# Optimization experiments

Measured on AMD Instinct MI355X. Metric: run time of the kernel, lower is better.

Reference implementation:

```python
import jax, jax.numpy as jnp
import numpy as np

B, S, D, H = 2, 2048, 1024, 16
DK = D // H  # 64


def setup_inputs() -> dict:
    key = jax.random.key(0)
    ks = jax.random.split(key, 12)
    def lin(kw, kb, fan_in, shape_w):
        bound = 1.0 / np.sqrt(fan_in)
        W = jax.random.uniform(kw, shape_w, jnp.float32, -bound, bound)
        b = jax.random.uniform(kb, (shape_w[0],), jnp.float32, -bound, bound)
        return W, b
    Q = jax.random.normal(ks[0], (B, S, D), jnp.float32)
    K = jax.random.normal(ks[1], (B, S, D), jnp.float32)
    V = jax.random.normal(ks[2], (B, S, D), jnp.float32)
    attn_mask = jax.random.randint(ks[3], (B, S, S), 0, 2) == 1  # bool, True=masked
    Wq, bq = lin(ks[4], ks[5], D, (D, D))
    Wk, bk = lin(ks[6], ks[7], D, (D, D))
    Wv, bv = lin(ks[8], ks[9], D, (D, D))
    Wo, bo = lin(ks[10], ks[11], D, (D, D))
    return {"Q": Q, "K": K, "V": V, "attn_mask": attn_mask,
            "Wq": Wq, "bq": bq, "Wk": Wk, "bk": bk,
            "Wv": Wv, "bv": bv, "Wo": Wo, "bo": bo}


def reference(Q, K, V, attn_mask, Wq, bq, Wk, bk, Wv, bv, Wo, bo):
    b, s, d = Q.shape
    # project and split heads: [B,S,D] -> [B,H,S,DK]
    def heads(x, W, bias):
        y = x @ W.T + bias
        return y.reshape(b, -1, H, DK).transpose(0, 2, 1, 3)
    q = heads(Q, Wq, bq)
    k = heads(K, Wk, bk)
    v = heads(V, Wv, bv)
    # scaled dot-product attention with custom reweighting
    scores = jnp.einsum('bhqd,bhkd->bhqk', q, k) / np.sqrt(DK).astype(jnp.float32)
    scores = jnp.where(attn_mask[:, None, :, :], jnp.float32(-1e9), scores)
    attn_weights = jax.nn.softmax(scores, axis=-1) * scores.shape[-1]  # non-standard *S_k scale
    ctx = jnp.einsum('bhqk,bhkd->bhqd', attn_weights, v)
    ctx = ctx.transpose(0, 2, 1, 3).reshape(b, -1, H * DK)
    output = ctx @ Wo.T + bo
    return output, attn_weights
```

## Files before the change

kernel.cpp:

```cpp
#include <hip/hip_runtime.h>
#include <hip/hip_bf16.h>
#include <type_traits>

typedef __bf16 bf16_t;
typedef __attribute__((ext_vector_type(8))) __bf16 bf16x8;
typedef __attribute__((ext_vector_type(4))) float f32x4;

#define B_ 2
#define S_ 2048
#define D_ 1024
#define H_ 16
#define DK_ 64

enum { OM_F32 = 0, OM_BF16 = 1, OM_SPLIT = 2, OM_HEADT = 3 };

__device__ inline void split8(const float* __restrict__ p, bf16x8& h, bf16x8& l) {
    float4 x0 = *(const float4*)p;
    float4 x1 = *(const float4*)(p + 4);
    float xs[8] = {x0.x, x0.y, x0.z, x0.w, x1.x, x1.y, x1.z, x1.w};
#pragma unroll
    for (int i = 0; i < 8; ++i) {
        bf16_t hh = (bf16_t)xs[i];
        h[i] = hh;
        l[i] = (bf16_t)(xs[i] - (float)hh);
    }
}
__device__ inline void hi8(const float* __restrict__ p, bf16x8& h) {
    float4 x0 = *(const float4*)p;
    float4 x1 = *(const float4*)(p + 4);
    float xs[8] = {x0.x, x0.y, x0.z, x0.w, x1.x, x1.y, x1.z, x1.w};
#pragma unroll
    for (int i = 0; i < 8; ++i) h[i] = (bf16_t)xs[i];
}

template <typename AT, int OMODE, bool SPLIT>
__global__ __launch_bounds__(256) void gemm_bt(
    const AT* __restrict__ A,
    const float* __restrict__ W,
    const float* __restrict__ bias,
    void* __restrict__ Yp,
    void* __restrict__ Y2p,
    int M, int N, int K)
{
    const int NB = N >> 6;
    const int bm = blockIdx.x / NB;
    const int bn = blockIdx.x % NB;
    const int tid  = threadIdx.x;
    const int wave = tid >> 6;
    const int lane = tid & 63;
    const int l16  = lane & 15;
    const int quad = lane >> 4;
    const int wm = wave >> 1, wn = wave & 1;

    __shared__ bf16_t Ah[64][40];
    __shared__ bf16_t Wh[64][40];
    __shared__ bf16_t Al[SPLIT ? 64 : 1][40];
    __shared__ bf16_t Wl[SPLIT ? 64 : 1][40];
    __shared__ bf16_t T[OMODE == OM_HEADT ? 64 : 1][72];

    const int srow = tid >> 2;
    const int scol = (tid & 3) * 8;

    f32x4 acc[2][2];
#pragma unroll
    for (int i = 0; i < 2; ++i)
#pragma unroll
        for (int j = 0; j < 2; ++j) acc[i][j] = (f32x4){0.f, 0.f, 0.f, 0.f};

    const AT*    Arow = A + (size_t)(bm * 64 + srow) * K + scol;
    const float* Wrow = W + (size_t)(bn * 64 + srow) * K + scol;

    for (int k0 = 0; k0 < K; k0 += 32) {
        if constexpr (std::is_same_v<AT, float>) {
            bf16x8 ah, al;
            if constexpr (SPLIT) {
                split8(Arow + k0, ah, al);
                *(bf16x8*)(&Al[srow][scol]) = al;
            } else {
                hi8(Arow + k0, ah);
            }
            *(bf16x8*)(&Ah[srow][scol]) = ah;
        } else {
            *(bf16x8*)(&Ah[srow][scol]) = *(const bf16x8*)(Arow + k0);
        }
        {
            bf16x8 wh, wl;
            if constexpr (SPLIT) {
                split8(Wrow + k0, wh, wl);
                *(bf16x8*)(&Wl[srow][scol]) = wl;
            } else {
                hi8(Wrow + k0, wh);
            }
            *(bf16x8*)(&Wh[srow][scol]) = wh;
        }
        __syncthreads();

        bf16x8 afh[2], bfh[2], afl[2], bfl[2];
#pragma unroll
        for (int mi = 0; mi < 2; ++mi) {
            afh[mi] = *(const bf16x8*)(&Ah[wm * 32 + mi * 16 + l16][quad * 8]);
            if constexpr (SPLIT)
                afl[mi] = *(const bf16x8*)(&Al[wm * 32 + mi * 16 + l16][quad * 8]);
        }
#pragma unroll
        for (int ni = 0; ni < 2; ++ni) {
            bfh[ni] = *(const bf16x8*)(&Wh[wn * 32 + ni * 16 + l16][quad * 8]);
            if constexpr (SPLIT)
                bfl[ni] = *(const bf16x8*)(&Wl[wn * 32 + ni * 16 + l16][quad * 8]);
        }

#pragma unroll
        for (int mi = 0; mi < 2; ++mi)
#pragma unroll
            for (int ni = 0; ni < 2; ++ni) {
                acc[mi][ni] = __builtin_amdgcn_mfma_f32_16x16x32_bf16(
                    afh[mi], bfh[ni], acc[mi][ni], 0, 0, 0);
                if constexpr (SPLIT) {
                    acc[mi][ni] = __builtin_amdgcn_mfma_f32_16x16x32_bf16(
                        afl[mi], bfh[ni], acc[mi][ni], 0, 0, 0);
                    acc[mi][ni] = __builtin_amdgcn_mfma_f32_16x16x32_bf16(
                        afh[mi], bfl[ni], acc[mi][ni], 0, 0, 0);
                }
            }
        __syncthreads();
    }

    if constexpr (OMODE == OM_HEADT) {
#pragma unroll
        for (int ni = 0; ni < 2; ++ni) {
            const int cl = wn * 32 + ni * 16 + l16;
            const float bv = bias[bn * 64 + cl];
#pragma unroll
            for (int mi = 0; mi < 2; ++mi)
#pragma unroll
                for (int r = 0; r < 4; ++r) {
                    const int rl = wm * 32 + mi * 16 + quad * 4 + r;
                    T[cl][rl] = (bf16_t)(acc[mi][ni][r] + bv);
                }
        }
        __syncthreads();
        const int bb  = bm >> 5;
        const int ss0 = (bm * 64) & (S_ - 1);
#pragma unroll
        for (int it = 0; it < 2; ++it) {
            const int dk = it * 32 + (tid >> 3);
            const int so = (tid & 7) * 8;
            *(bf16x8*)((bf16_t*)Yp +
                ((size_t)((bb * H_ + bn) * DK_ + dk) << 11) + ss0 + so) =
                *(const bf16x8*)(&T[dk][so]);
        }
        return;
    }

#pragma unroll
    for (int ni = 0; ni < 2; ++ni) {
        const int col = bn * 64 + wn * 32 + ni * 16 + l16;
        const float bv = bias[col];
#pragma unroll
        for (int mi = 0; mi < 2; ++mi) {
#pragma unroll
            for (int r = 0; r < 4; ++r) {
                const int row = bm * 64 + wm * 32 + mi * 16 + quad * 4 + r;
                const float v = acc[mi][ni][r] + bv;
                if constexpr (OMODE == OM_F32) {
                    ((float*)Yp)[(size_t)row * N + col] = v;
                } else if constexpr (OMODE == OM_BF16) {
                    ((bf16_t*)Yp)[(size_t)row * N + col] = (bf16_t)v;
                } else if constexpr (OMODE == OM_SPLIT) {
                    const bf16_t hh = (bf16_t)v;
                    ((bf16_t*)Yp)[(size_t)row * N + col] = hh;
                    ((bf16_t*)Y2p)[(size_t)row * N + col] = (bf16_t)(v - (float)hh);
                }
            }
        }
    }
}

__global__ __launch_bounds__(256) void pack_mask(
    const int* __restrict__ mask,
    unsigned long long* __restrict__ pk)
{
    const size_t nwords = (size_t)B_ * S_ * S_ / 64;
    const int lane = threadIdx.x & 63;
    size_t w = (size_t)blockIdx.x * 4 + (threadIdx.x >> 6);
    const size_t stride = (size_t)gridDim.x * 4;
    for (; w < nwords; w += stride) {
        const int m = mask[w * 64 + lane];
        const unsigned long long bb = __ballot(m != 0);
        if (lane == 0) pk[w] = bb;
    }
}

__global__ __launch_bounds__(256) void attn_scores(
    const bf16_t* __restrict__ qh_g,
    const bf16_t* __restrict__ ql_g,
    const bf16_t* __restrict__ kh_g,
    const bf16_t* __restrict__ kl_g,
    const unsigned long long* __restrict__ pm,
    float* __restrict__ wout,
    float* __restrict__ normbuf)
{
    const int bid = blockIdx.x;
    const int qt = bid & 31;
    const int h  = (bid >> 5) & 15;
    const int b  = bid >> 9;
    const int tid  = threadIdx.x;
    const int wave = tid >> 6;
    const int lane = tid & 63;
    const int l16  = lane & 15;
    const int quad = lane >> 4;

    const int q0 = qt * 64 + wave * 16;

    __shared__ bf16_t Kh[64][72];
    __shared__ bf16_t Kl[64][72];

    const size_t qoff = ((size_t)(b * S_ + q0 + l16)) * D_ + h * DK_ + quad * 8;
    const bf16x8 qh0 = *(const bf16x8*)(qh_g + qoff);
    const bf16x8 qh1 = *(const bf16x8*)(qh_g + qoff + 32);
    const bf16x8 ql0 = *(const bf16x8*)(ql_g + qoff);
    const bf16x8 ql1 = *(const bf16x8*)(ql_g + qoff + 32);

    const float scale = 0.125f;

    const int srow = tid >> 2;
    const int scol = (tid & 3) * 16;
    const bf16_t* khst = kh_g + (size_t)b * S_ * D_ + h * DK_;
    const bf16_t* klst = kl_g + (size_t)b * S_ * D_ + h * DK_;

    const unsigned long long* pmrow = pm + (size_t)b * S_ * (S_ / 64);
    const size_t wbase = ((size_t)(b * H_ + h)) * S_ * S_;

    float lsum[4] = {0.f, 0.f, 0.f, 0.f};

    for (int j0 = 0; j0 < S_; j0 += 64) {
        {
            const size_t ko = (size_t)(j0 + srow) * D_ + scol;
            *(bf16x8*)(&Kh[srow][scol])     = *(const bf16x8*)(khst + ko);
            *(bf16x8*)(&Kh[srow][scol + 8]) = *(const bf16x8*)(khst + ko + 8);
            *(bf16x8*)(&Kl[srow][scol])     = *(const bf16x8*)(klst + ko);
            *(bf16x8*)(&Kl[srow][scol + 8]) = *(const bf16x8*)(klst + ko + 8);
        }
        unsigned long long mw[4];
#pragma unroll
        for (int r = 0; r < 4; ++r) {
            const int q = q0 + quad * 4 + r;
            mw[r] = pmrow[(size_t)q * (S_ / 64) + (j0 >> 6)];
        }
        __syncthreads();

#pragma unroll
        for (int sub = 0; sub < 4; ++sub) {
            const int rr = sub * 16 + l16;
            const bf16x8 kh0 = *(const bf16x8*)(&Kh[rr][quad * 8]);
            const bf16x8 kh1 = *(const bf16x8*)(&Kh[rr][32 + quad * 8]);
            const bf16x8 kl0 = *(const bf16x8*)(&Kl[rr][quad * 8]);
            const bf16x8 kl1 = *(const bf16x8*)(&Kl[rr][32 + quad * 8]);
            f32x4 c = (f32x4){0.f, 0.f, 0.f, 0.f};
            c = __builtin_amdgcn_mfma_f32_16x16x32_bf16(qh0, kh0, c, 0, 0, 0);
            c = __builtin_amdgcn_mfma_f32_16x16x32_bf16(qh1, kh1, c, 0, 0, 0);
            c = __builtin_amdgcn_mfma_f32_16x16x32_bf16(ql0, kh0, c, 0, 0, 0);
            c = __builtin_amdgcn_mfma_f32_16x16x32_bf16(ql1, kh1, c, 0, 0, 0);
            c = __builtin_amdgcn_mfma_f32_16x16x32_bf16(qh0, kl0, c, 0, 0, 0);
            c = __builtin_amdgcn_mfma_f32_16x16x32_bf16(qh1, kl1, c, 0, 0, 0);
            const int jt = j0 + sub * 16;
#pragma unroll
            for (int r = 0; r < 4; ++r) {
                const int q = q0 + quad * 4 + r;
                const int msk = (int)((mw[r] >> (sub * 16 + l16)) & 1ull);
                const float e = msk ? 0.f : __expf(c[r] * scale);
                lsum[r] += e;
                __builtin_nontemporal_store(e, &wout[wbase + (size_t)q * S_ + jt + l16]);
            }
        }
        __syncthreads();
    }

#pragma unroll
    for (int r = 0; r < 4; ++r) {
        float v = lsum[r];
        v += __shfl_xor(v, 1);
        v += __shfl_xor(v, 2);
        v += __shfl_xor(v, 4);
        v += __shfl_xor(v, 8);
        lsum[r] = v;
    }
    if (l16 == 0) {
#pragma unroll
        for (int r = 0; r < 4; ++r)
            normbuf[(size_t)(b * H_ + h) * S_ + q0 + quad * 4 + r] = 2048.f / lsum[r];
    }
}

__global__ __launch_bounds__(256) void attn_pv(
    const bf16_t* __restrict__ vt_g,
    const float*  __restrict__ normbuf,
    float* __restrict__ wout,
    bf16_t* __restrict__ ctx)
{
    const int bid = blockIdx.x;
    const int qt = bid & 31;
    const int h  = (bid >> 5) & 15;
    const int b  = bid >> 9;
    const int tid  = threadIdx.x;
    const int wave = tid >> 6;
    const int lane = tid & 63;
    const int l16  = lane & 15;
    const int quad = lane >> 4;

    const int q0 = qt * 64 + wave * 16;

    __shared__ bf16_t vT[64][72];

    const int sdk = tid >> 2;
    const int sjo = (tid & 3) * 16;
    const bf16_t* vtst = vt_g + ((size_t)(b * H_ + h) * DK_ + sdk) * S_ + sjo;

    const size_t wbase = ((size_t)(b * H_ + h)) * S_ * S_;
    const float nrmA = normbuf[(size_t)(b * H_ + h) * S_ + q0 + l16];
    float norm_c[4];
#pragma unroll
    for (int r = 0; r < 4; ++r)
        norm_c[r] = normbuf[(size_t)(b * H_ + h) * S_ + q0 + quad * 4 + r];

    f32x4 acc[4];
#pragma unroll
    for (int t = 0; t < 4; ++t) acc[t] = (f32x4){0.f, 0.f, 0.f, 0.f};

    float* wrow = wout + wbase + (size_t)(q0 + l16) * S_;

    for (int j0 = 0; j0 < S_; j0 += 64) {
        {
            *(bf16x8*)(&vT[sdk][sjo])     = *(const bf16x8*)(vtst + j0);
            *(bf16x8*)(&vT[sdk][sjo + 8]) = *(const bf16x8*)(vtst + j0 + 8);
        }
        __syncthreads();

#pragma unroll
        for (int half = 0; half < 2; ++half) {
            const int jj = j0 + half * 32 + quad * 8;
            float* ep = wrow + jj;
            float4 e0, e1;
            e0.x = __builtin_nontemporal_load(ep + 0);
            e0.y = __builtin_nontemporal_load(ep + 1);
            e0.z = __builtin_nontemporal_load(ep + 2);
            e0.w = __builtin_nontemporal_load(ep + 3);
            e1.x = __builtin_nontemporal_load(ep + 4);
            e1.y = __builtin_nontemporal_load(ep + 5);
            e1.z = __builtin_nontemporal_load(ep + 6);
            e1.w = __builtin_nontemporal_load(ep + 7);
            const float es[8] = {e0.x, e0.y, e0.z, e0.w, e1.x, e1.y, e1.z, e1.w};
            bf16x8 wa;
#pragma unroll
            for (int i = 0; i < 8; ++i) {
                __builtin_nontemporal_store(es[i] * nrmA, ep + i);
                wa[i] = (bf16_t)es[i];
            }
#pragma unroll
            for (int t = 0; t < 4; ++t) {
                const bf16x8 vf = *(const bf16x8*)(&vT[t * 16 + l16][half * 32 + quad * 8]);
                acc[t] = __builtin_amdgcn_mfma_f32_16x16x32_bf16(wa, vf, acc[t], 0, 0, 0);
            }
        }
        __syncthreads();
    }

#pragma unroll
    for (int t = 0; t < 4; ++t) {
#pragma unroll
        for (int r = 0; r < 4; ++r) {
            const int q = q0 + quad * 4 + r;
            ctx[((size_t)(b * S_ + q)) * D_ + h * DK_ + t * 16 + l16] =
                (bf16_t)(acc[t][r] * norm_c[r]);
        }
    }
}

extern "C" void kernel_launch(void* const* d_in, const int* in_sizes, int n_in,
                              void* d_out, int out_size, void* d_ws, size_t ws_size,
                              hipStream_t stream) {
    const float* Q    = (const float*)d_in[0];
    const float* K    = (const float*)d_in[1];
    const float* V    = (const float*)d_in[2];
    const int*   mask = (const int*)d_in[3];
    const float* Wq   = (const float*)d_in[4];
    const float* bq   = (const float*)d_in[5];
    const float* Wk   = (const float*)d_in[6];
    const float* bk   = (const float*)d_in[7];
    const float* Wv   = (const float*)d_in[8];
    const float* bv   = (const float*)d_in[9];
    const float* Wo   = (const float*)d_in[10];
    const float* bo   = (const float*)d_in[11];

    const size_t BSD = (size_t)B_ * S_ * D_;
    float* out  = (float*)d_out;
    float* wout = out + BSD;

    bf16_t* qh = (bf16_t*)d_ws;
    bf16_t* ql = qh + BSD;
    bf16_t* kh = ql + BSD;
    bf16_t* kl = kh + BSD;
    bf16_t* vt = kl + BSD;
    bf16_t* cx = vt + BSD;
    unsigned long long* pk = (unsigned long long*)(cx + BSD);
    float* normbuf = (float*)(pk + (size_t)B_ * S_ * (S_ / 64));

    const int M = B_ * S_;
    const int N = D_;
    const int Kd = D_;
    const dim3 ggrid((M / 64) * (N / 64));
    const dim3 gblk(256);

    pack_mask<<<dim3(512), gblk, 0, stream>>>(mask, pk);

    gemm_bt<float, OM_SPLIT, true><<<ggrid, gblk, 0, stream>>>(Q, Wq, bq, qh, ql, M, N, Kd);
    gemm_bt<float, OM_SPLIT, true><<<ggrid, gblk, 0, stream>>>(K, Wk, bk, kh, kl, M, N, Kd);
    gemm_bt<float, OM_HEADT, false><<<ggrid, gblk, 0, stream>>>(V, Wv, bv, vt, nullptr, M, N, Kd);

    attn_scores<<<dim3(B_ * H_ * (S_ / 64)), gblk, 0, stream>>>(
        qh, ql, kh, kl, pk, wout, normbuf);

    attn_pv<<<dim3(B_ * H_ * (S_ / 64)), gblk, 0, stream>>>(
        vt, normbuf, wout, cx);

    gemm_bt<bf16_t, OM_F32, false><<<ggrid, gblk, 0, stream>>>(cx, Wo, bo, out, nullptr, M, N, Kd);
}
```

Baseline: 1.130 ms.

## Fuse attention scores and PV into two-pass kernel recomputing QK

```diff
diff --git a/kernel.cpp b/kernel.cpp
--- a/kernel.cpp
+++ b/kernel.cpp
@@ -191,14 +191,15 @@
     }
 }
 
-__global__ __launch_bounds__(256) void attn_scores(
+__global__ __launch_bounds__(256) void attn_kernel(
     const bf16_t* __restrict__ qh_g,
     const bf16_t* __restrict__ ql_g,
     const bf16_t* __restrict__ kh_g,
     const bf16_t* __restrict__ kl_g,
+    const bf16_t* __restrict__ vt_g,
     const unsigned long long* __restrict__ pm,
     float* __restrict__ wout,
-    float* __restrict__ normbuf)
+    bf16_t* __restrict__ ctx)
 {
     const int bid = blockIdx.x;
     const int qt = bid & 31;
@@ -214,6 +215,8 @@
 
     __shared__ bf16_t Kh[64][72];
     __shared__ bf16_t Kl[64][72];
+    __shared__ bf16_t vT[64][72];
+    __shared__ bf16_t wl[4][16][72];
 
     const size_t qoff = ((size_t)(b * S_ + q0 + l16)) * D_ + h * DK_ + quad * 8;
     const bf16x8 qh0 = *(const bf16x8*)(qh_g + qoff);
@@ -227,6 +230,7 @@
     const int scol = (tid & 3) * 16;
     const bf16_t* khst = kh_g + (size_t)b * S_ * D_ + h * DK_;
     const bf16_t* klst = kl_g + (size_t)b * S_ * D_ + h * DK_;
+    const bf16_t* vtst = vt_g + ((size_t)(b * H_ + h) * DK_ + srow) * S_ + scol;
 
     const unsigned long long* pmrow = pm + (size_t)b * S_ * (S_ / 64);
     const size_t wbase = ((size_t)(b * H_ + h)) * S_ * S_;
@@ -240,6 +244,64 @@
             *(bf16x8*)(&Kh[srow][scol + 8]) = *(const bf16x8*)(khst + ko + 8);
             *(bf16x8*)(&Kl[srow][scol])     = *(const bf16x8*)(klst + ko);
             *(bf16x8*)(&Kl[srow][scol + 8]) = *(const bf16x8*)(klst + ko + 8);
+        }
+        unsigned long long mw[4];
+#pragma unroll
+        for (int r = 0; r < 4; ++r) {
+            const int q = q0 + quad * 4 + r;
+            mw[r] = pmrow[(size_t)q * (S_ / 64) + (j0 >> 6)];
+        }
+        __syncthreads();
+
+#pragma unroll
+        for (int sub = 0; sub < 4; ++sub) {
+            const int rr = sub * 16 + l16;
+            const bf16x8 kh0 = *(const bf16x8*)(&Kh[rr][quad * 8]);
+            const bf16x8 kh1 = *(const bf16x8*)(&Kh[rr][32 + quad * 8]);
+            const bf16x8 kl0 = *(const bf16x8*)(&Kl[rr][quad * 8]);
+            const bf16x8 kl1 = *(const bf16x8*)(&Kl[rr][32 + quad * 8]);
+            f32x4 c = (f32x4){0.f, 0.f, 0.f, 0.f};
+            c = __builtin_amdgcn_mfma_f32_16x16x32_bf16(qh0, kh0, c, 0, 0, 0);
+            c = __builtin_amdgcn_mfma_f32_16x16x32_bf16(qh1, kh1, c, 0, 0, 0);
+            c = __builtin_amdgcn_mfma_f32_16x16x32_bf16(ql0, kh0, c, 0, 0, 0);
+            c = __builtin_amdgcn_mfma_f32_16x16x32_bf16(ql1, kh1, c, 0, 0, 0);
+            c = __builtin_amdgcn_mfma_f32_16x16x32_bf16(qh0, kl0, c, 0, 0, 0);
+            c = __builtin_amdgcn_mfma_f32_16x16x32_bf16(qh1, kl1, c, 0, 0, 0);
+#pragma unroll
+            for (int r = 0; r < 4; ++r) {
+                const int msk = (int)((mw[r] >> (sub * 16 + l16)) & 1ull);
+                lsum[r] += msk ? 0.f : __expf(c[r] * scale);
+            }
+        }
+        __syncthreads();
+    }
+
+#pragma unroll
+    for (int r = 0; r < 4; ++r) {
+        float v = lsum[r];
+        v += __shfl_xor(v, 1);
+        v += __shfl_xor(v, 2);
+        v += __shfl_xor(v, 4);
+        v += __shfl_xor(v, 8);
+        lsum[r] = v;
+    }
+    float norm[4];
+#pragma unroll
+    for (int r = 0; r < 4; ++r) norm[r] = 2048.f / lsum[r];
+
+    f32x4 acc[4];
+#pragma unroll
+    for (int t = 0; t < 4; ++t) acc[t] = (f32x4){0.f, 0.f, 0.f, 0.f};
+
+    for (int j0 = 0; j0 < S_; j0 += 64) {
+        {
+            const size_t ko = (size_t)(j0 + srow) * D_ + scol;
+            *(bf16x8*)(&Kh[srow][scol])     = *(const bf16x8*)(khst + ko);
+            *(bf16x8*)(&Kh[srow][scol + 8]) = *(const bf16x8*)(khst + ko + 8);
+            *(bf16x8*)(&Kl[srow][scol])     = *(const bf16x8*)(klst + ko);
+            *(bf16x8*)(&Kl[srow][scol + 8]) = *(const bf16x8*)(klst + ko + 8);
+            *(bf16x8*)(&vT[srow][scol])     = *(const bf16x8*)(vtst + j0);
+            *(bf16x8*)(&vT[srow][scol + 8]) = *(const bf16x8*)(vtst + j0 + 8);
         }
         unsigned long long mw[4];
 #pragma unroll
@@ -269,98 +331,19 @@
                 const int q = q0 + quad * 4 + r;
                 const int msk = (int)((mw[r] >> (sub * 16 + l16)) & 1ull);
                 const float e = msk ? 0.f : __expf(c[r] * scale);
-                lsum[r] += e;
-                __builtin_nontemporal_store(e, &wout[wbase + (size_t)q * S_ + jt + l16]);
-            }
-        }
-        __syncthreads();
-    }
-
-#pragma unroll
-    for (int r = 0; r < 4; ++r) {
-        float v = lsum[r];
-        v += __shfl_xor(v, 1);
-        v += __shfl_xor(v, 2);
-        v += __shfl_xor(v, 4);
-        v += __shfl_xor(v, 8);
-        lsum[r] = v;
-    }
-    if (l16 == 0) {
-#pragma unroll
-        for (int r = 0; r < 4; ++r)
-            normbuf[(size_t)(b * H_ + h) * S_ + q0 + quad * 4 + r] = 2048.f / lsum[r];
-    }
-}
-
-__global__ __launch_bounds__(256) void attn_pv(
-    const bf16_t* __restrict__ vt_g,
-    const float*  __restrict__ normbuf,
-    float* __restrict__ wout,
-    bf16_t* __restrict__ ctx)
-{
-    const int bid = blockIdx.x;
-    const int qt = bid & 31;
-    const int h  = (bid >> 5) & 15;
-    const int b  = bid >> 9;
-    const int tid  = threadIdx.x;
-    const int wave = tid >> 6;
-    const int lane = tid & 63;
-    const int l16  = lane & 15;
-    const int quad = lane >> 4;
-
-    const int q0 = qt * 64 + wave * 16;
-
-    __shared__ bf16_t vT[64][72];
-
-    const int sdk = tid >> 2;
-    const int sjo = (tid & 3) * 16;
-    const bf16_t* vtst = vt_g + ((size_t)(b * H_ + h) * DK_ + sdk) * S_ + sjo;
-
-    const size_t wbase = ((size_t)(b * H_ + h)) * S_ * S_;
-    const float nrmA = normbuf[(size_t)(b * H_ + h) * S_ + q0 + l16];
-    float norm_c[4];
-#pragma unroll
-    for (int r = 0; r < 4; ++r)
-        norm_c[r] = normbuf[(size_t)(b * H_ + h) * S_ + q0 + quad * 4 + r];
-
-    f32x4 acc[4];
-#pragma unroll
-    for (int t = 0; t < 4; ++t) acc[t] = (f32x4){0.f, 0.f, 0.f, 0.f};
-
-    float* wrow = wout + wbase + (size_t)(q0 + l16) * S_;
-
-    for (int j0 = 0; j0 < S_; j0 += 64) {
-        {
-            *(bf16x8*)(&vT[sdk][sjo])     = *(const bf16x8*)(vtst + j0);
-            *(bf16x8*)(&vT[sdk][sjo + 8]) = *(const bf16x8*)(vtst + j0 + 8);
-        }
-        __syncthreads();
-
-#pragma unroll
-        for (int half = 0; half < 2; ++half) {
-            const int jj = j0 + half * 32 + quad * 8;
-            float* ep = wrow + jj;
-            float4 e0, e1;
-            e0.x = __builtin_nontemporal_load(ep + 0);
-            e0.y = __builtin_nontemporal_load(ep + 1);
-            e0.z = __builtin_nontemporal_load(ep + 2);
-            e0.w = __builtin_nontemporal_load(ep + 3);
-            e1.x = __builtin_nontemporal_load(ep + 4);
-            e1.y = __builtin_nontemporal_load(ep + 5);
-            e1.z = __builtin_nontemporal_load(ep + 6);
-            e1.w = __builtin_nontemporal_load(ep + 7);
-            const float es[8] = {e0.x, e0.y, e0.z, e0.w, e1.x, e1.y, e1.z, e1.w};
-            bf16x8 wa;
-#pragma unroll
-            for (int i = 0; i < 8; ++i) {
-                __builtin_nontemporal_store(es[i] * nrmA, ep + i);
-                wa[i] = (bf16_t)es[i];
-            }
-#pragma unroll
-            for (int t = 0; t < 4; ++t) {
-                const bf16x8 vf = *(const bf16x8*)(&vT[t * 16 + l16][half * 32 + quad * 8]);
-                acc[t] = __builtin_amdgcn_mfma_f32_16x16x32_bf16(wa, vf, acc[t], 0, 0, 0);
-            }
+                __builtin_nontemporal_store(e * norm[r],
+                    &wout[wbase + (size_t)q * S_ + jt + l16]);
+                wl[wave][quad * 4 + r][sub * 16 + l16] = (bf16_t)e;
+            }
+        }
+        const bf16x8 wa0 = *(const bf16x8*)(&wl[wave][l16][quad * 8]);
+        const bf16x8 wa1 = *(const bf16x8*)(&wl[wave][l16][32 + quad * 8]);
+#pragma unroll
+        for (int t = 0; t < 4; ++t) {
+            const bf16x8 vf0 = *(const bf16x8*)(&vT[t * 16 + l16][quad * 8]);
+            const bf16x8 vf1 = *(const bf16x8*)(&vT[t * 16 + l16][32 + quad * 8]);
+            acc[t] = __builtin_amdgcn_mfma_f32_16x16x32_bf16(wa0, vf0, acc[t], 0, 0, 0);
+            acc[t] = __builtin_amdgcn_mfma_f32_16x16x32_bf16(wa1, vf1, acc[t], 0, 0, 0);
         }
         __syncthreads();
     }
@@ -371,7 +354,7 @@
         for (int r = 0; r < 4; ++r) {
             const int q = q0 + quad * 4 + r;
             ctx[((size_t)(b * S_ + q)) * D_ + h * DK_ + t * 16 + l16] =
-                (bf16_t)(acc[t][r] * norm_c[r]);
+                (bf16_t)(acc[t][r] * norm[r]);
         }
     }
 }
@@ -403,7 +386,6 @@
     bf16_t* vt = kl + BSD;
     bf16_t* cx = vt + BSD;
     unsigned long long* pk = (unsigned long long*)(cx + BSD);
-    float* normbuf = (float*)(pk + (size_t)B_ * S_ * (S_ / 64));
 
     const int M = B_ * S_;
     const int N = D_;
@@ -417,11 +399,8 @@
     gemm_bt<float, OM_SPLIT, true><<<ggrid, gblk, 0, stream>>>(K, Wk, bk, kh, kl, M, N, Kd);
     gemm_bt<float, OM_HEADT, false><<<ggrid, gblk, 0, stream>>>(V, Wv, bv, vt, nullptr, M, N, Kd);
 
-    attn_scores<<<dim3(B_ * H_ * (S_ / 64)), gblk, 0, stream>>>(
-        qh, ql, kh, kl, pk, wout, normbuf);
-
-    attn_pv<<<dim3(B_ * H_ * (S_ / 64)), gblk, 0, stream>>>(
-        vt, normbuf, wout, cx);
+    attn_kernel<<<dim3(B_ * H_ * (S_ / 64)), gblk, 0, stream>>>(
+        qh, ql, kh, kl, vt, pk, wout, cx);
 
     gemm_bt<bf16_t, OM_F32, false><<<ggrid, gblk, 0, stream>>>(cx, Wo, bo, out, nullptr, M, N, Kd);
 }
```

New measurement: 929.4 us. 1.22x faster.
